# Optimization experiments

Hardware: AMD Instinct MI355X
Metric: run time of the kernel (lower is better)

Reference implementation:

```python
import jax, jax.numpy as jnp
import numpy as np
from jax import lax

N, IC, OC, K, SDIM, H, W = 16, 512, 512, 3, 512, 32, 32
PAD, STRIDE, LR = 1, 1, 1.0
WEIGHT_SCALER = 1.0 / np.sqrt(IC * K * K) * LR   # equalized-lr conv scale
FC_SCALER = 1.0 / np.sqrt(SDIM) * LR             # equalized-lr fc scale


def setup_inputs() -> dict:
    key = jax.random.key(0)
    k1, k2, k3 = jax.random.split(key, 3)
    x = jax.random.normal(k1, (N, IC, H, W), dtype=jnp.float32)
    style = jax.random.normal(k2, (N, SDIM), dtype=jnp.float32)
    weight = jax.random.normal(k3, (OC, IC, K, K), dtype=jnp.float32)  # std = 1/lr = 1
    fc_weight = jax.random.normal(jax.random.fold_in(key, 10), (IC, SDIM), dtype=jnp.float32)
    fc_bias = jnp.zeros((IC,), dtype=jnp.float32)
    return {"x": x, "style": style, "weight": weight,
            "fc_weight": fc_weight, "fc_bias": fc_bias}


def reference(x, style, weight, fc_weight, fc_bias):
    # EqualizedFullyConnect + AddChannelwiseBias, then +1 -> modulation rates [N, iC]
    mod = jnp.einsum('ns,cs->nc', style, fc_weight) * FC_SCALER + fc_bias * LR + 1.0
    # modulated per-sample weight [N, oC, iC, kH, kW]
    w = WEIGHT_SCALER * weight[None] * mod[:, None, :, None, None]
    # demodulate: rsqrt of sum of squares over (iC, kH, kW)
    demod = lax.rsqrt(jnp.sum(w * w, axis=(2, 3, 4)) + 1e-8)  # [N, oC]
    w = w * demod[:, :, None, None, None]
    # grouped conv with groups=N == per-sample conv: vmap over batch
    def conv1(xi, wi):
        # xi: [iC,H,W], wi: [oC,iC,kH,kW]
        return lax.conv_general_dilated(
            xi[None], wi, window_strides=(STRIDE, STRIDE),
            padding=((PAD, PAD), (PAD, PAD)),
            dimension_numbers=('NCHW', 'OIHW', 'NCHW'))[0]
    out = jax.vmap(conv1)(x, w)  # [N, oC, H, W]
    return out
```

## Files before the change

### kernel.cpp

```cpp
#include <hip/hip_runtime.h>
#include <hip/hip_bf16.h>

#define N_    16
#define IC_   512
#define OC_   512
#define SDIM_ 512
#define H_    32
#define W_    32
#define HW_   1024

#define FC_SCALER 0.04419417382415922f
#define WS_       0.014731391274719738f
#define WS2_      (1.0f/4608.0f)

typedef __attribute__((__ext_vector_type__(8)))  __bf16 bf16x8;
typedef __attribute__((__ext_vector_type__(16))) float  f32x16;
typedef __attribute__((__ext_vector_type__(4)))  int    i32x4;

typedef __attribute__((address_space(1))) const unsigned int GInt;
typedef __attribute__((address_space(3))) unsigned int LInt;

#define WAIT12() asm volatile("s_waitcnt vmcnt(12)" ::: "memory")
#define WAIT0()  asm volatile("s_waitcnt vmcnt(0)"  ::: "memory")
#define LGKM0()  asm volatile("s_waitcnt lgkmcnt(0)" ::: "memory")
#define SB()     __builtin_amdgcn_sched_barrier(0)

__device__ __forceinline__ unsigned short f2bf(float f) {
    unsigned int u = __builtin_bit_cast(unsigned int, f);
    unsigned int r = (u + 0x7FFFu + ((u >> 16) & 1u)) >> 16;
    return (unsigned short)r;
}

__global__ void k_mod(const float* __restrict__ style, const float* __restrict__ fcw,
                      const float* __restrict__ fcb, float* __restrict__ mod) {
    int gid = blockIdx.x * blockDim.x + threadIdx.x;
    int wid = gid >> 6, lane = gid & 63;
    if (wid >= N_ * IC_) return;
    int n = wid >> 9, c = wid & 511;
    const float4* sp = (const float4*)(style + n * SDIM_);
    const float4* wp = (const float4*)(fcw + (size_t)c * SDIM_);
    float acc = 0.f;
    for (int i = lane; i < SDIM_ / 4; i += 64) {
        float4 a = sp[i], b = wp[i];
        acc += a.x*b.x + a.y*b.y + a.z*b.z + a.w*b.w;
    }
#pragma unroll
    for (int off = 32; off; off >>= 1) acc += __shfl_xor(acc, off);
    if (lane == 0) mod[wid] = acc * FC_SCALER + fcb[c] + 1.0f;
}

__global__ void k_wprep(const float* __restrict__ w, unsigned short* __restrict__ wt,
                        float* __restrict__ wsq) {
    int tid = blockIdx.x * blockDim.x + threadIdx.x;
    int oc = tid >> 9, ic = tid & 511;
    int og = oc >> 6, ocl = oc & 63;
    int icc = ic >> 5, ks = (ic >> 3) & 3, i8 = ic & 7;
    float s = 0.f;
#pragma unroll
    for (int t = 0; t < 9; t++) {
        float v = w[(size_t)tid * 9 + t];
        s += v * v;
        size_t off = (((size_t)t * 8 + og) * 16 + icc) * 2048
                   + (size_t)ks * 512 + ocl * 8 + i8;
        wt[off] = f2bf(v);
    }
    wsq[tid] = s;
}

__global__ void k_demod(const float* __restrict__ mod, const float* __restrict__ wsq,
                        float* __restrict__ demod_ws) {
    int gid = blockIdx.x * blockDim.x + threadIdx.x;
    int wid = gid >> 6, lane = gid & 63;
    if (wid >= N_ * OC_) return;
    int n = wid >> 9, oc = wid & 511;
    const float4* mp = (const float4*)(mod + n * IC_);
    const float4* qp = (const float4*)(wsq + (size_t)oc * IC_);
    float acc = 0.f;
    for (int i = lane; i < IC_ / 4; i += 64) {
        float4 m = mp[i], q = qp[i];
        acc += m.x*m.x*q.x + m.y*m.y*q.y + m.z*m.z*q.z + m.w*m.w*q.w;
    }
#pragma unroll
    for (int off = 32; off; off >>= 1) acc += __shfl_xor(acc, off);
    if (lane == 0) {
        float s = WS2_ * acc + 1e-8f;
        demod_ws[wid] = WS_ / sqrtf(s);
    }
}

__global__ void k_premod(const float* __restrict__ x, const float* __restrict__ mod,
                         unsigned short* __restrict__ xm) {
    __shared__ __align__(16) unsigned short t_lds[64][80];
    int bx = blockIdx.x;
    int n = bx >> 7, hwt = (bx >> 3) & 15, ict = bx & 7;
    int hw0 = hwt * 64, ic0 = ict * 64;
    int tid = threadIdx.x, lane = tid & 63, ty = tid >> 6;
#pragma unroll
    for (int jj = 0; jj < 16; jj++) {
        int icl = ty * 16 + jj;
        float v = x[(size_t)(n * IC_ + ic0 + icl) * HW_ + hw0 + lane]
                  * mod[n * IC_ + ic0 + icl];
        t_lds[lane][icl] = f2bf(v);
    }
    __syncthreads();
    int xcol = tid & 31, ks64 = tid >> 5;
    int icc = ict * 2 + (ks64 >> 2), ks = ks64 & 3;
#pragma unroll
    for (int rep = 0; rep < 2; rep++) {
        int hwl = rep * 32 + xcol;
        i32x4 v = *(const i32x4*)&t_lds[hwl][ks64 * 8];
        int y = (hw0 >> 5) + rep;
        size_t off = ((((size_t)n * 16 + icc) * 32 + y) * 4 + ks) * 256 + xcol * 8;
        *(i32x4*)(xm + off) = v;
    }
}

__global__ __launch_bounds__(256, 2)
void k_conv(const unsigned short* __restrict__ xm, const unsigned short* __restrict__ wt,
            const float* __restrict__ demod_ws, float* __restrict__ out) {
    __shared__ __align__(16) char smem[42304];
    unsigned short* xt0     = (unsigned short*)(smem);
    unsigned short* trash   = (unsigned short*)(smem + 40960);
    float*          zslot   = (float*)(smem + 41984);
    float*          s_demod = (float*)(smem + 42016);

    int bx = blockIdx.x;
    int xcd = bx & 7, j = bx >> 3;
    int h = xcd & 1, q = xcd >> 1;
    int a = j >> 4, b = (j >> 2) & 3, s = j & 3;
    int octg = h * 4 + a, n = q * 4 + b, spt = s;
    int oc0 = octg * 64, y0 = spt * 8;

    int tid = threadIdx.x, lane = tid & 63, wid = tid >> 6;
    int l31 = lane & 31, lhi = lane >> 5;
    int wc = wid & 1, kh = wid >> 1;
    int kso = kh * 2 + lhi;

    if (tid < 64) s_demod[tid] = demod_ws[n * OC_ + oc0 + tid];
    if (tid == 0) { i32x4 z = {}; *(i32x4*)zslot = z; }
    if (spt == 0 && tid < 128) {
        i32x4 z = {};
        *(i32x4*)&xt0[tid * 8] = z;
        *(i32x4*)&xt0[10240 + tid * 8] = z;
    }
    if (spt == 3 && tid < 128) {
        i32x4 z = {};
        *(i32x4*)&xt0[9 * 1024 + tid * 8] = z;
        *(i32x4*)&xt0[10240 + 9 * 1024 + tid * 8] = z;
    }
    WAIT0();
    SB();

    const unsigned short* xsrc_n = xm + (size_t)n * (16 * 32 * 1024);

    auto stage_x = [&](int buf, int icc) {
#pragma unroll
        for (int k = 0; k < 5; k++) {
            int c = wid + k * 4;
            int rr = c >> 1, hh = c & 1;
            int y = y0 - 1 + rr;
            bool oob = ((unsigned)y >= 32u) | (icc >= 16);
            int yc = y < 0 ? 0 : (y > 31 ? 31 : y);
            int iccc = icc & 15;
            const unsigned short* g =
                xsrc_n + ((size_t)iccc * 32 + yc) * 1024 + hh * 512 + lane * 8;
            unsigned short* l = oob ? trash
                                    : xt0 + buf * 10240 + rr * 1024 + hh * 512;
            __builtin_amdgcn_global_load_lds((GInt*)g, (LInt*)l, 16, 0, 0);
        }
    };
    auto fetch_A = [&](int g2, bf16x8 (&dst)[6]) {
        int gc = g2 < 48 ? g2 : 47;
        int icc2 = gc / 3, p2 = gc - icc2 * 3;
#pragma unroll
        for (int dy = 0; dy < 3; dy++) {
            int tap = dy * 3 + p2;
            const unsigned short* base =
                wt + (((size_t)tap * 8 + octg) * 16 + icc2) * 2048 + kso * 512 + l31 * 8;
            dst[dy * 2 + 0] = *(const bf16x8*)(base);
            dst[dy * 2 + 1] = *(const bf16x8*)(base + 256);
        }
    };

    f32x16 acc[2][4] = {};
    int xb = 0;

    auto compute = [&](int p, const bf16x8 (&wAv)[6]) {
        const unsigned short* xtb = xt0 + xb * 10240;
        int col = l31 + p - 1;
        bool oobc = (unsigned)col >= 32u;
        bf16x8 r6[6];
#pragma unroll
        for (int jj2 = 0; jj2 < 6; jj2++) {
            int rr = wc * 4 + jj2;
            const unsigned short* src = oobc ? (const unsigned short*)zslot
                : xtb + rr * 1024 + kso * 256 + col * 8;
            r6[jj2] = *(const bf16x8*)src;
        }
#pragma unroll
        for (int dy = 0; dy < 3; dy++) {
            __builtin_amdgcn_s_setprio(1);
#pragma unroll
            for (int fs = 0; fs < 4; fs++)
                acc[0][fs] = __builtin_amdgcn_mfma_f32_32x32x16_bf16(
                    wAv[dy * 2 + 0], r6[fs + dy], acc[0][fs], 0, 0, 0);
#pragma unroll
            for (int fs = 0; fs < 4; fs++)
                acc[1][fs] = __builtin_amdgcn_mfma_f32_32x32x16_bf16(
                    wAv[dy * 2 + 1], r6[fs + dy], acc[1][fs], 0, 0, 0);
            __builtin_amdgcn_s_setprio(0);
        }
    };

    bf16x8 wS0[6], wS1[6], wS2[6];

    stage_x(0, 0);
    fetch_A(0, wS0);
    fetch_A(1, wS1);
    LGKM0();

#pragma unroll 1
    for (int icc = 0; icc < 16; icc++) {
        int g0 = icc * 3;
        WAIT12();
        __builtin_amdgcn_s_barrier();
        SB();
        fetch_A(g0 + 2, wS2);
        stage_x(xb ^ 1, icc + 1);
        SB();
        compute(0, wS0);
        SB();
        fetch_A(g0 + 3, wS0);
        SB();
        compute(1, wS1);
        SB();
        fetch_A(g0 + 4, wS1);
        SB();
        compute(2, wS2);
        SB();
        xb ^= 1;
    }

    WAIT0();
    __syncthreads();
    float* exch = (float*)smem;
#pragma unroll
    for (int fo = 0; fo < 2; fo++) {
        if (kh == 1) {
#pragma unroll
            for (int fs = 0; fs < 4; fs++)
#pragma unroll
                for (int rg = 0; rg < 16; rg++)
                    exch[((wc * 4 + fs) * 16 + rg) * 64 + lane] = acc[fo][fs][rg];
        }
        __syncthreads();
        if (kh == 0) {
#pragma unroll
            for (int fs = 0; fs < 4; fs++) {
                int y = y0 + wc * 4 + fs;
#pragma unroll
                for (int rg = 0; rg < 16; rg++) {
                    int row = (rg & 3) + 8 * (rg >> 2) + 4 * lhi;
                    int ocl = fo * 32 + row;
                    float v = acc[fo][fs][rg]
                            + exch[((wc * 4 + fs) * 16 + rg) * 64 + lane];
                    v *= s_demod[ocl];
                    out[((size_t)(n * OC_ + oc0 + ocl) * H_ + y) * W_ + l31] = v;
                }
            }
        }
        __syncthreads();
    }
}

extern "C" void kernel_launch(void* const* d_in, const int* in_sizes, int n_in,
                              void* d_out, int out_size, void* d_ws, size_t ws_size,
                              hipStream_t stream) {
    const float* x      = (const float*)d_in[0];
    const float* style  = (const float*)d_in[1];
    const float* weight = (const float*)d_in[2];
    const float* fcw    = (const float*)d_in[3];
    const float* fcb    = (const float*)d_in[4];
    float* out = (float*)d_out;

    char* ws = (char*)d_ws;
    float*          mod   = (float*)ws;
    float*          demod = (float*)(ws + 32768);
    float*          wsq   = (float*)(ws + 65536);
    unsigned short* wtb   = (unsigned short*)(ws + 65536 + 1048576);
    unsigned short* xmb   = (unsigned short*)(ws + 65536 + 1048576 + 4718592);

    k_mod   <<<2048, 256, 0, stream>>>(style, fcw, fcb, mod);
    k_wprep <<<1024, 256, 0, stream>>>(weight, wtb, wsq);
    k_demod <<<2048, 256, 0, stream>>>(mod, wsq, demod);
    k_premod<<<2048, 256, 0, stream>>>(x, mod, xmb);
    k_conv  <<<512,  256, 0, stream>>>(xmb, wtb, demod, out);
}
```

Before: 101.8 us.

## Restructure inner loop with two weight buffers and prefetched LDS reads

Splits the compute step into a separate LDS read and an MFMA cluster, so input rows for the next tap are read from LDS while the current MFMA cluster runs. Weight fragments now rotate through two register buffers instead of three, with the loop unrolled by two to swap them. Odd-numbered groups of blocks also sleep briefly at start, which staggers their memory traffic. The trade-off is that each weight fragment is fetched shortly before use, so global latency may be exposed, and one fetch per iteration is redundant.

Result: slower. 173.7 us (+70.5%).

```diff
diff --git a/kernel.cpp b/kernel.cpp
--- a/kernel.cpp
+++ b/kernel.cpp
@@ -185,11 +185,10 @@
     f32x16 acc[2][4] = {};
     int xb = 0;
 
-    auto compute = [&](int p, const bf16x8 (&wAv)[6]) {
+    auto read_r6 = [&](int p, bf16x8 (&r6)[6]) {
         const unsigned short* xtb = xt0 + xb * 10240;
         int col = l31 + p - 1;
         bool oobc = (unsigned)col >= 32u;
-        bf16x8 r6[6];
 #pragma unroll
         for (int jj2 = 0; jj2 < 6; jj2++) {
             int rr = wc * 4 + jj2;
@@ -197,48 +196,62 @@
                 : xtb + rr * 1024 + kso * 256 + col * 8;
             r6[jj2] = *(const bf16x8*)src;
         }
+    };
+    auto mfma_cluster = [&](const bf16x8 (&wS)[6], const bf16x8 (&r6)[6]) {
 #pragma unroll
         for (int dy = 0; dy < 3; dy++) {
             __builtin_amdgcn_s_setprio(1);
 #pragma unroll
             for (int fs = 0; fs < 4; fs++)
                 acc[0][fs] = __builtin_amdgcn_mfma_f32_32x32x16_bf16(
-                    wAv[dy * 2 + 0], r6[fs + dy], acc[0][fs], 0, 0, 0);
+                    wS[dy * 2 + 0], r6[fs + dy], acc[0][fs], 0, 0, 0);
 #pragma unroll
             for (int fs = 0; fs < 4; fs++)
                 acc[1][fs] = __builtin_amdgcn_mfma_f32_32x32x16_bf16(
-                    wAv[dy * 2 + 1], r6[fs + dy], acc[1][fs], 0, 0, 0);
+                    wS[dy * 2 + 1], r6[fs + dy], acc[1][fs], 0, 0, 0);
             __builtin_amdgcn_s_setprio(0);
         }
     };
 
-    bf16x8 wS0[6], wS1[6], wS2[6];
+    bf16x8 wSa[6], wSb[6], rA[6], rB[6];
 
     stage_x(0, 0);
-    fetch_A(0, wS0);
-    fetch_A(1, wS1);
+    fetch_A(0, wSa);
+    fetch_A(1, wSb);
     LGKM0();
-
-#pragma unroll 1
-    for (int icc = 0; icc < 16; icc++) {
+    if ((bx >> 8) & 1) __builtin_amdgcn_s_sleep(32);
+
+    auto icc_body = [&](int icc, bf16x8 (&sE)[6], bf16x8 (&sO)[6]) {
         int g0 = icc * 3;
         WAIT12();
         __builtin_amdgcn_s_barrier();
         SB();
-        fetch_A(g0 + 2, wS2);
+        read_r6(0, rA);
+        SB();
+        fetch_A(g0 + 1, sO);
         stage_x(xb ^ 1, icc + 1);
         SB();
-        compute(0, wS0);
-        SB();
-        fetch_A(g0 + 3, wS0);
-        SB();
-        compute(1, wS1);
-        SB();
-        fetch_A(g0 + 4, wS1);
-        SB();
-        compute(2, wS2);
+        read_r6(1, rB);
+        SB();
+        mfma_cluster(sE, rA);
+        SB();
+        read_r6(2, rA);
+        SB();
+        fetch_A(g0 + 2, sE);
+        SB();
+        mfma_cluster(sO, rB);
+        SB();
+        fetch_A(g0 + 3, sO);
+        SB();
+        mfma_cluster(sE, rA);
         SB();
         xb ^= 1;
+    };
+
+#pragma unroll 1
+    for (int ii = 0; ii < 8; ii++) {
+        icc_body(2 * ii,     wSa, wSb);
+        icc_body(2 * ii + 1, wSb, wSa);
     }
 
     WAIT0();
```
